# Kernel tuning notes

Measured on AMD Instinct MI355X. Metric: run time of the kernel, lower is better.

Reference implementation:

```python
import jax, jax.numpy as jnp
import numpy as np

EPS = 1e-5


def _rmsnorm(x, eps=EPS):
    return x * jax.lax.rsqrt(jnp.mean(x * x, axis=-1, keepdims=True) + eps)


def _bitlinear(x, w):
    # fla-style BitLinear: RMSNorm (no affine) -> 8-bit activation quant (STE)
    # -> ternary weight quant (STE) -> linear. w is [out, in].
    xn = _rmsnorm(x)
    s = 127.0 / jnp.clip(jnp.max(jnp.abs(xn), axis=-1, keepdims=True), 1e-5, None)
    xq = jnp.clip(jnp.round(xn * s), -128.0, 127.0) / s
    xq = xn + jax.lax.stop_gradient(xq - xn)
    ws = 1.0 / jnp.clip(jnp.mean(jnp.abs(w)), 1e-5, None)
    wq = jnp.clip(jnp.round(w * ws), -1.0, 1.0) / ws
    wq = w + jax.lax.stop_gradient(wq - w)
    return jnp.einsum('bld,od->blo', xq, wq)


def _hgrn_scan(i, f):
    # h_t = f_t * h_{t-1} + i_t along axis=2 (seq), h_0 = 0.
    def combine(a, b):
        fa, ia = a
        fb, ib = b
        return fa * fb, ia * fb + ib
    _, h = jax.lax.associative_scan(combine, (f, i), axis=2)
    return h


def _forward(hidden_states, Wi, Wf, Wg, Wo, g_norm_weight, num_heads=1):
    b, l, d = hidden_states.shape
    i = _bitlinear(hidden_states, Wi)
    f = jax.nn.sigmoid(_bitlinear(hidden_states, Wf))
    i = jax.nn.silu(i) * (1.0 - f)  # swiglu(i, 1-f)
    # [b, l, (h d)] -> [b, h, l, d_head]
    i = i.reshape(b, l, num_heads, -1).transpose(0, 2, 1, 3)
    f = f.reshape(b, l, num_heads, -1).transpose(0, 2, 1, 3)
    h = _hgrn_scan(i, f)
    h = h.transpose(0, 2, 1, 3).reshape(b, l, d)
    # FusedRMSNormSwishGate: rmsnorm(g)*weight * h*sigmoid(h)
    g = _bitlinear(hidden_states, Wg)
    o = _rmsnorm(g) * g_norm_weight * (h * jax.nn.sigmoid(h))
    return _bitlinear(o, Wo)


def setup_inputs() -> dict:
    key = jax.random.key(0)
    ks = jax.random.split(key, 5)
    B, L, D = 4, 2048, 2048
    gain = 2 ** (-2.5) * (6.0 / (2 * D)) ** 0.5  # xavier_uniform with gain 2^-2.5
    def w(k):
        return jax.random.uniform(k, (D, D), jnp.float32, -gain, gain)
    return {
        'hidden_states': jax.random.normal(ks[0], (B, L, D), jnp.float32),
        'Wi': w(ks[1]),
        'Wf': w(ks[2]),
        'Wg': w(ks[3]),
        'Wo': w(ks[4]),
        'g_norm_weight': jnp.ones((D,), jnp.float32),
    }


def reference(hidden_states, Wi, Wf, Wg, Wo, g_norm_weight):
    return _forward(hidden_states, Wi, Wf, Wg, Wo, g_norm_weight)
```

## Files before the change

### kernel.cpp

```cpp
#include <hip/hip_runtime.h>
#include <stdint.h>

#define B_DIM 4
#define L_DIM 2048
#define D_DIM 2048
#define M_DIM 8192
#define K_DIM 2048
#define N_DIM 2048
#define WELEM (D_DIM * D_DIM)
#define CHUNK 32
#define NCH (L_DIM / CHUNK)

typedef int v4i __attribute__((ext_vector_type(4)));
typedef unsigned short bfraw;

#define AS1 __attribute__((address_space(1)))
#define AS3 __attribute__((address_space(3)))

__device__ __forceinline__ void gl_lds16(const void* g, void* l) {
    __builtin_amdgcn_global_load_lds((AS1 void*)g, (AS3 void*)l, 16, 0, 0);
}

__device__ __forceinline__ float sigmoidf_(float x) { return 1.0f / (1.0f + expf(-x)); }

__device__ __forceinline__ float bf2f(bfraw u) {
    union { unsigned int i; float f; } c; c.i = ((unsigned int)u) << 16; return c.f;
}
__device__ __forceinline__ bfraw f2bf(float f) {
    union { float f; unsigned int i; } c; c.f = f;
    unsigned int lsb = (c.i >> 16) & 1;
    c.i += 0x7fffu + lsb;
    return (bfraw)(c.i >> 16);
}

__device__ __forceinline__ void store_out(float* p, float v) { *p = v; }
__device__ __forceinline__ void store_out(bfraw* p, float v) { *p = f2bf(v); }

__device__ __forceinline__ float block_sum256(float v) {
#pragma unroll
    for (int off = 32; off > 0; off >>= 1) v += __shfl_down(v, off);
    __shared__ float sb[4];
    int lane = threadIdx.x & 63, wv = threadIdx.x >> 6;
    __syncthreads();
    if (lane == 0) sb[wv] = v;
    __syncthreads();
    return sb[0] + sb[1] + sb[2] + sb[3];
}

__device__ __forceinline__ void block_sum_max256(float& s, float& m) {
#pragma unroll
    for (int off = 32; off > 0; off >>= 1) {
        s += __shfl_down(s, off);
        m = fmaxf(m, __shfl_down(m, off));
    }
    __shared__ float sb2[8];
    int lane = threadIdx.x & 63, wv = threadIdx.x >> 6;
    __syncthreads();
    if (lane == 0) { sb2[wv] = s; sb2[4 + wv] = m; }
    __syncthreads();
    s = sb2[0] + sb2[1] + sb2[2] + sb2[3];
    m = fmaxf(fmaxf(sb2[4], sb2[5]), fmaxf(sb2[6], sb2[7]));
}

__global__ void wstats1(const float* __restrict__ w0, const float* __restrict__ w1,
                        const float* __restrict__ w2, const float* __restrict__ w3,
                        float* __restrict__ wpart) {
    int w = blockIdx.x >> 7;
    int slice = blockIdx.x & 127;
    const float* W = (w == 0) ? w0 : ((w == 1) ? w1 : ((w == 2) ? w2 : w3));
    const float4* p = (const float4*)(W + (size_t)slice * (WELEM / 128));
    float s = 0.f;
    for (int i = threadIdx.x; i < (WELEM / 128 / 4); i += 256) {
        float4 v = p[i];
        s += fabsf(v.x) + fabsf(v.y) + fabsf(v.z) + fabsf(v.w);
    }
    s = block_sum256(s);
    if (threadIdx.x == 0) wpart[blockIdx.x] = s;
}

__global__ void wstats2(const float* __restrict__ wpart, float* __restrict__ wdeq) {
    int w = threadIdx.x >> 6;
    int lane = threadIdx.x & 63;
    float s = wpart[w * 128 + lane] + wpart[w * 128 + 64 + lane];
#pragma unroll
    for (int off = 32; off > 0; off >>= 1) s += __shfl_down(s, off);
    if (lane == 0) wdeq[w] = fmaxf(s * (1.0f / (float)WELEM), 1e-5f);
}

__global__ void quant_all(const float* __restrict__ w0, const float* __restrict__ w1,
                          const float* __restrict__ w2, const float* __restrict__ w3,
                          const float* __restrict__ wdeq, int8_t* __restrict__ wq,
                          const float* __restrict__ x, int8_t* __restrict__ xq,
                          float* __restrict__ adeq) {
    if (blockIdx.x < 16384) {
        size_t idx = (size_t)blockIdx.x * 256 + threadIdx.x;
        int w = (int)(idx >> 20);
        size_t g = idx & ((1u << 20) - 1);
        const float* W = (w == 0) ? w0 : ((w == 1) ? w1 : ((w == 2) ? w2 : w3));
        float inv = 1.0f / wdeq[w];
        float4 v = ((const float4*)W)[g];
        int q0 = (int)rintf(v.x * inv); q0 = q0 < -1 ? -1 : (q0 > 1 ? 1 : q0);
        int q1 = (int)rintf(v.y * inv); q1 = q1 < -1 ? -1 : (q1 > 1 ? 1 : q1);
        int q2 = (int)rintf(v.z * inv); q2 = q2 < -1 ? -1 : (q2 > 1 ? 1 : q2);
        int q3 = (int)rintf(v.w * inv); q3 = q3 < -1 ? -1 : (q3 > 1 ? 1 : q3);
        uint32_t p = (uint32_t)(q0 & 0xff) | ((uint32_t)(q1 & 0xff) << 8) |
                     ((uint32_t)(q2 & 0xff) << 16) | ((uint32_t)(q3 & 0xff) << 24);
        ((uint32_t*)(wq + (size_t)w * WELEM))[g] = p;
        return;
    }
    int row = blockIdx.x - 16384, tid = threadIdx.x;
    const float4* xr = (const float4*)(x + (size_t)row * D_DIM);
    float4 a = xr[2 * tid], b = xr[2 * tid + 1];
    float v[8] = {a.x, a.y, a.z, a.w, b.x, b.y, b.z, b.w};
    float ss = 0.f, mx = 0.f;
#pragma unroll
    for (int j = 0; j < 8; j++) { ss += v[j] * v[j]; mx = fmaxf(mx, fabsf(v[j])); }
    block_sum_max256(ss, mx);
    float inv = rsqrtf(ss * (1.0f / (float)D_DIM) + 1e-5f);
    float anc = fmaxf(mx * inv, 1e-5f);
    float s = 127.0f / anc;
    if (tid == 0) adeq[row] = anc * (1.0f / 127.0f);
    float sc = inv * s;
    int q[8];
#pragma unroll
    for (int j = 0; j < 8; j++) {
        int t = (int)rintf(v[j] * sc);
        q[j] = t < -128 ? -128 : (t > 127 ? 127 : t);
    }
    uint32_t lo = (uint32_t)(q[0] & 0xff) | ((uint32_t)(q[1] & 0xff) << 8) |
                  ((uint32_t)(q[2] & 0xff) << 16) | ((uint32_t)(q[3] & 0xff) << 24);
    uint32_t hi = (uint32_t)(q[4] & 0xff) | ((uint32_t)(q[5] & 0xff) << 8) |
                  ((uint32_t)(q[6] & 0xff) << 16) | ((uint32_t)(q[7] & 0xff) << 24);
    ((uint2*)(xq + (size_t)row * D_DIM))[tid] = make_uint2(lo, hi);
}

#define BM 128
#define BN 256
#define BKB 64

template <typename OutT>
__device__ __forceinline__ void gemm_core(
    const int8_t* __restrict__ A, const int8_t* __restrict__ Bw,
    const float* __restrict__ adeq, float wsc,
    int m0, int n0, OutT* __restrict__ Cout) {
    __shared__ int8_t sA[BM * BKB];
    __shared__ int8_t sB[BN * BKB];
    int lane = threadIdx.x & 63;
    int wv = threadIdx.x >> 6;
    int wm = (wv & 1) * 64;
    int wn = (wv >> 1) * 128;

    const v4i vzero = {0, 0, 0, 0};
    v4i acc[4][8];
#pragma unroll
    for (int i = 0; i < 4; i++)
#pragma unroll
        for (int j = 0; j < 8; j++) acc[i][j] = vzero;

    int rS = lane >> 2;
    int cS = (lane & 3) * 16;
    const int8_t* Ablk = A + (size_t)m0 * K_DIM;
    const int8_t* Bblk = Bw + (size_t)n0 * K_DIM;
    int qq = lane >> 4;
    int mr = lane & 15;

    for (int kt = 0; kt < K_DIM; kt += BKB) {
        gl_lds16(Ablk + (size_t)(wv * 16 + rS) * K_DIM + kt + cS, sA + (wv * 16) * BKB);
        gl_lds16(Ablk + (size_t)(64 + wv * 16 + rS) * K_DIM + kt + cS, sA + (64 + wv * 16) * BKB);
#pragma unroll
        for (int g = 0; g < 4; g++) {
            int rb = g * 64 + wv * 16;
            gl_lds16(Bblk + (size_t)(rb + rS) * K_DIM + kt + cS, sB + rb * BKB);
        }
        __syncthreads();

        v4i afrag[4], bfrag[8];
#pragma unroll
        for (int i = 0; i < 4; i++)
            afrag[i] = *(const v4i*)(sA + (size_t)(wm + i * 16 + mr) * BKB + qq * 16);
#pragma unroll
        for (int j = 0; j < 8; j++)
            bfrag[j] = *(const v4i*)(sB + (size_t)(wn + j * 16 + mr) * BKB + qq * 16);
#pragma unroll
        for (int i = 0; i < 4; i++)
#pragma unroll
            for (int j = 0; j < 8; j++)
                acc[i][j] = __builtin_amdgcn_mfma_i32_16x16x64_i8(afrag[i], bfrag[j], acc[i][j], 0, 0, 0);
        __syncthreads();
    }

    int cc = lane & 15;
#pragma unroll
    for (int i = 0; i < 4; i++) {
#pragma unroll
        for (int r = 0; r < 4; r++) {
            int row = m0 + wm + i * 16 + qq * 4 + r;
            float rs = adeq[row] * wsc;
            OutT* crow = Cout + (size_t)row * N_DIM + n0 + wn + cc;
#pragma unroll
            for (int j = 0; j < 8; j++) store_out(crow + j * 16, (float)acc[i][j][r] * rs);
        }
    }
}

__global__ __launch_bounds__(256, 2) void gemm_ifg(
    const int8_t* __restrict__ xq, const int8_t* __restrict__ wq,
    const float* __restrict__ adeq, const float* __restrict__ wdeq,
    bfraw* __restrict__ bufI, bfraw* __restrict__ bufF, bfraw* __restrict__ bufG) {
    int widx = blockIdx.x >> 3;
    int n0 = (blockIdx.x & 7) * BN;
    int m0 = blockIdx.y * BM;
    bfraw* outp = (widx == 0) ? bufI : ((widx == 1) ? bufF : bufG);
    gemm_core<bfraw>(xq, wq + (size_t)widx * WELEM, adeq, wdeq[widx], m0, n0, outp);
}

__global__ __launch_bounds__(256, 2) void gemm_o(
    const int8_t* __restrict__ oq, const int8_t* __restrict__ wq,
    const float* __restrict__ odeq, const float* __restrict__ wdeq,
    float* __restrict__ out) {
    gemm_core<float>(oq, wq + 3 * (size_t)WELEM, odeq, wdeq[3], blockIdx.y * BM,
                     blockIdx.x * BN, out);
}

__global__ void scan1(const bfraw* __restrict__ iL, const bfraw* __restrict__ fL,
                      float* __restrict__ Fc, float* __restrict__ Ic) {
    int idx = blockIdx.x * 256 + threadIdx.x;
    int d = idx & (D_DIM - 1);
    int c = (idx >> 11) & (NCH - 1);
    int b = idx >> 17;
    size_t base = ((size_t)(b * L_DIM + c * CHUNK)) * D_DIM + d;
    float F = 1.f, h = 0.f;
#pragma unroll 4
    for (int t = 0; t < CHUNK; t++) {
        float fr = bf2f(fL[base + (size_t)t * D_DIM]);
        float ir = bf2f(iL[base + (size_t)t * D_DIM]);
        float fv = sigmoidf_(fr);
        float iv = ir * sigmoidf_(ir) * (1.0f - fv);
        h = fv * h + iv;
        F *= fv;
    }
    size_t ci = ((size_t)b * NCH + c) * D_DIM + d;
    Fc[ci] = F;
    Ic[ci] = h;
}

__global__ void scan2(const float* __restrict__ Fc, const float* __restrict__ Ic,
                      float* __restrict__ Hc) {
    int idx = blockIdx.x * 256 + threadIdx.x;
    int d = idx & (D_DIM - 1);
    int b = idx >> 11;
    float h = 0.f;
    for (int c0 = 0; c0 < NCH; c0 += 8) {
        float F[8], I[8];
#pragma unroll
        for (int j = 0; j < 8; j++) {
            size_t ci = ((size_t)b * NCH + c0 + j) * D_DIM + d;
            F[j] = Fc[ci];
            I[j] = Ic[ci];
        }
#pragma unroll
        for (int j = 0; j < 8; j++) {
            size_t ci = ((size_t)b * NCH + c0 + j) * D_DIM + d;
            Hc[ci] = h;
            h = F[j] * h + I[j];
        }
    }
}

__global__ void scan3(const bfraw* __restrict__ iL, const bfraw* __restrict__ fL,
                      const float* __restrict__ Hc, bfraw* __restrict__ hout) {
    int idx = blockIdx.x * 256 + threadIdx.x;
    int d = idx & (D_DIM - 1);
    int c = (idx >> 11) & (NCH - 1);
    int b = idx >> 17;
    size_t base = ((size_t)(b * L_DIM + c * CHUNK)) * D_DIM + d;
    float h = Hc[((size_t)b * NCH + c) * D_DIM + d];
#pragma unroll 4
    for (int t = 0; t < CHUNK; t++) {
        size_t a = base + (size_t)t * D_DIM;
        float fr = bf2f(fL[a]);
        float ir = bf2f(iL[a]);
        float fv = sigmoidf_(fr);
        float iv = ir * sigmoidf_(ir) * (1.0f - fv);
        h = fv * h + iv;
        hout[a] = f2bf(h);
    }
}

union BF8 { uint4 u; bfraw s[8]; };

__global__ void gout_quant(const bfraw* __restrict__ gL, const bfraw* __restrict__ h,
                           const float* __restrict__ gw, int8_t* __restrict__ oq,
                           float* __restrict__ odeq) {
    int row = blockIdx.x, tid = threadIdx.x;
    BF8 g8, h8;
    g8.u = ((const uint4*)(gL + (size_t)row * D_DIM))[tid];
    float gv[8];
    float ss = 0.f;
#pragma unroll
    for (int j = 0; j < 8; j++) { gv[j] = bf2f(g8.s[j]); ss += gv[j] * gv[j]; }
    float ssg = block_sum256(ss);
    float invg = rsqrtf(ssg * (1.0f / (float)D_DIM) + 1e-5f);

    h8.u = ((const uint4*)(h + (size_t)row * D_DIM))[tid];
    const float4* wr = (const float4*)gw;
    float4 w0 = wr[2 * tid], w1 = wr[2 * tid + 1];
    float wv[8] = {w0.x, w0.y, w0.z, w0.w, w1.x, w1.y, w1.z, w1.w};
    float o[8];
    float sso = 0.f, amax = 0.f;
#pragma unroll
    for (int j = 0; j < 8; j++) {
        float hv = bf2f(h8.s[j]);
        o[j] = gv[j] * invg * wv[j] * hv * sigmoidf_(hv);
        sso += o[j] * o[j];
        amax = fmaxf(amax, fabsf(o[j]));
    }
    block_sum_max256(sso, amax);
    float invo = rsqrtf(sso * (1.0f / (float)D_DIM) + 1e-5f);
    float anc = fmaxf(amax * invo, 1e-5f);
    float s = 127.0f / anc;
    if (tid == 0) odeq[row] = anc * (1.0f / 127.0f);
    float sc = invo * s;
    int q[8];
#pragma unroll
    for (int j = 0; j < 8; j++) {
        int t = (int)rintf(o[j] * sc);
        q[j] = t < -128 ? -128 : (t > 127 ? 127 : t);
    }
    uint32_t lo = (uint32_t)(q[0] & 0xff) | ((uint32_t)(q[1] & 0xff) << 8) |
                  ((uint32_t)(q[2] & 0xff) << 16) | ((uint32_t)(q[3] & 0xff) << 24);
    uint32_t hi = (uint32_t)(q[4] & 0xff) | ((uint32_t)(q[5] & 0xff) << 8) |
                  ((uint32_t)(q[6] & 0xff) << 16) | ((uint32_t)(q[7] & 0xff) << 24);
    ((uint2*)(oq + (size_t)row * D_DIM))[tid] = make_uint2(lo, hi);
}

extern "C" void kernel_launch(void* const* d_in, const int* in_sizes, int n_in,
                              void* d_out, int out_size, void* d_ws, size_t ws_size,
                              hipStream_t stream) {
    const float* x  = (const float*)d_in[0];
    const float* Wi = (const float*)d_in[1];
    const float* Wf = (const float*)d_in[2];
    const float* Wg = (const float*)d_in[3];
    const float* Wo = (const float*)d_in[4];
    const float* gw = (const float*)d_in[5];
    float* out = (float*)d_out;

    char* ws = (char*)d_ws;
    float*  wdeq  = (float*)(ws + 0);
    float*  wpart = (float*)(ws + 256);
    float*  adeq  = (float*)(ws + 0x10000);
    float*  odeq  = (float*)(ws + 0x20000);
    int8_t* xq    = (int8_t*)(ws + 0x100000);
    int8_t* wq    = (int8_t*)(ws + 0x1100000);
    float*  Fc    = (float*)(ws + 0x2100000);
    float*  Ic    = (float*)(ws + 0x2300000);
    float*  Hc    = (float*)(ws + 0x2500000);
    bfraw*  bufI  = (bfraw*)(ws + 0x4000000);
    bfraw*  bufF  = (bfraw*)(ws + 0x6000000);
    bfraw*  bufG  = (bfraw*)(ws + 0x8000000);
    bfraw*  hbuf  = (bfraw*)(ws + 0xA000000);

    wstats1<<<512, 256, 0, stream>>>(Wi, Wf, Wg, Wo, wpart);
    wstats2<<<1, 256, 0, stream>>>(wpart, wdeq);
    quant_all<<<16384 + 8192, 256, 0, stream>>>(Wi, Wf, Wg, Wo, wdeq, wq, x, xq, adeq);

    gemm_ifg<<<dim3(24, M_DIM / BM), 256, 0, stream>>>(xq, wq, adeq, wdeq, bufI, bufF, bufG);

    scan1<<<2048, 256, 0, stream>>>(bufI, bufF, Fc, Ic);
    scan2<<<32, 256, 0, stream>>>(Fc, Ic, Hc);
    scan3<<<2048, 256, 0, stream>>>(bufI, bufF, Hc, hbuf);

    gout_quant<<<M_DIM, 256, 0, stream>>>(bufG, hbuf, gw, xq , odeq);
    gemm_o<<<dim3(N_DIM / BN, M_DIM / BM), 256, 0, stream>>>(xq , wq, odeq, wdeq, out);

    (void)in_sizes; (void)n_in; (void)out_size; (void)ws_size;
}
```

Measured before the change: 430.9 us.

## Fuse pipeline into one cooperative persistent kernel with grid syncs and swizzled LDS

All stages (weight stats, quantization, the three input GEMMs, the chunked scan, the gated norm plus quant, and the output GEMM) move into one cooperative persistent kernel with 512 or 256 blocks, separated by grid.sync. The separate kernels are kept as a fallback if the cooperative launch fails. The GEMM LDS layout also gets an XOR swizzle on 16-byte columns to reduce bank conflicts. This removes launch gaps between nine kernels, but the persistent grid caps GEMM parallelism at the resident block count, ties every stage to the GEMM's register and LDS footprint, and adds grid-sync cost.

```diff
diff --git a/kernel.cpp b/kernel.cpp
--- a/kernel.cpp
+++ b/kernel.cpp
@@ -1,5 +1,8 @@
 #include <hip/hip_runtime.h>
+#include <hip/hip_cooperative_groups.h>
 #include <stdint.h>
+
+namespace cg = cooperative_groups;
 
 #define B_DIM 4
 #define L_DIM 2048
@@ -11,6 +14,10 @@
 #define CHUNK 32
 #define NCH (L_DIM / CHUNK)
 
+#define BM 128
+#define BN 256
+#define BKB 64
+
 typedef int v4i __attribute__((ext_vector_type(4)));
 typedef unsigned short bfraw;
 
@@ -36,10 +43,9 @@
 __device__ __forceinline__ void store_out(float* p, float v) { *p = v; }
 __device__ __forceinline__ void store_out(bfraw* p, float v) { *p = f2bf(v); }
 
-__device__ __forceinline__ float block_sum256(float v) {
+__device__ __forceinline__ float block_sum256(float v, float* sb) {
 #pragma unroll
     for (int off = 32; off > 0; off >>= 1) v += __shfl_down(v, off);
-    __shared__ float sb[4];
     int lane = threadIdx.x & 63, wv = threadIdx.x >> 6;
     __syncthreads();
     if (lane == 0) sb[wv] = v;
@@ -47,57 +53,47 @@
     return sb[0] + sb[1] + sb[2] + sb[3];
 }
 
-__device__ __forceinline__ void block_sum_max256(float& s, float& m) {
+__device__ __forceinline__ void block_sum_max256(float& s, float& m, float* sb) {
 #pragma unroll
     for (int off = 32; off > 0; off >>= 1) {
         s += __shfl_down(s, off);
         m = fmaxf(m, __shfl_down(m, off));
     }
-    __shared__ float sb2[8];
     int lane = threadIdx.x & 63, wv = threadIdx.x >> 6;
     __syncthreads();
-    if (lane == 0) { sb2[wv] = s; sb2[4 + wv] = m; }
+    if (lane == 0) { sb[wv] = s; sb[4 + wv] = m; }
     __syncthreads();
-    s = sb2[0] + sb2[1] + sb2[2] + sb2[3];
-    m = fmaxf(fmaxf(sb2[4], sb2[5]), fmaxf(sb2[6], sb2[7]));
-}
-
-__global__ void wstats1(const float* __restrict__ w0, const float* __restrict__ w1,
-                        const float* __restrict__ w2, const float* __restrict__ w3,
-                        float* __restrict__ wpart) {
-    int w = blockIdx.x >> 7;
-    int slice = blockIdx.x & 127;
-    const float* W = (w == 0) ? w0 : ((w == 1) ? w1 : ((w == 2) ? w2 : w3));
+    s = sb[0] + sb[1] + sb[2] + sb[3];
+    m = fmaxf(fmaxf(sb[4], sb[5]), fmaxf(sb[6], sb[7]));
+}
+
+
+__device__ __forceinline__ void wstats1_body(int u, const float* Wi, const float* Wf,
+                                             const float* Wg, const float* Wo,
+                                             float* wpart, float* red) {
+    int w = u >> 7, slice = u & 127;
+    const float* W = (w == 0) ? Wi : ((w == 1) ? Wf : ((w == 2) ? Wg : Wo));
     const float4* p = (const float4*)(W + (size_t)slice * (WELEM / 128));
     float s = 0.f;
     for (int i = threadIdx.x; i < (WELEM / 128 / 4); i += 256) {
         float4 v = p[i];
         s += fabsf(v.x) + fabsf(v.y) + fabsf(v.z) + fabsf(v.w);
     }
-    s = block_sum256(s);
-    if (threadIdx.x == 0) wpart[blockIdx.x] = s;
-}
-
-__global__ void wstats2(const float* __restrict__ wpart, float* __restrict__ wdeq) {
-    int w = threadIdx.x >> 6;
-    int lane = threadIdx.x & 63;
-    float s = wpart[w * 128 + lane] + wpart[w * 128 + 64 + lane];
-#pragma unroll
-    for (int off = 32; off > 0; off >>= 1) s += __shfl_down(s, off);
-    if (lane == 0) wdeq[w] = fmaxf(s * (1.0f / (float)WELEM), 1e-5f);
-}
-
-__global__ void quant_all(const float* __restrict__ w0, const float* __restrict__ w1,
-                          const float* __restrict__ w2, const float* __restrict__ w3,
-                          const float* __restrict__ wdeq, int8_t* __restrict__ wq,
-                          const float* __restrict__ x, int8_t* __restrict__ xq,
-                          float* __restrict__ adeq) {
-    if (blockIdx.x < 16384) {
-        size_t idx = (size_t)blockIdx.x * 256 + threadIdx.x;
-        int w = (int)(idx >> 20);
-        size_t g = idx & ((1u << 20) - 1);
-        const float* W = (w == 0) ? w0 : ((w == 1) ? w1 : ((w == 2) ? w2 : w3));
-        float inv = 1.0f / wdeq[w];
+    s = block_sum256(s, red);
+    if (threadIdx.x == 0) wpart[u] = s;
+}
+
+__device__ __forceinline__ void quant_body(int unit, const float* Wi, const float* Wf,
+                                           const float* Wg, const float* Wo,
+                                           const float* wdq, int8_t* wq,
+                                           const float* x, int8_t* xq, float* adeq,
+                                           float* red) {
+    int tid = threadIdx.x;
+    if (unit < 16384) {
+        int w = unit >> 12;
+        size_t g = ((size_t)(unit & 4095)) * 256 + tid;
+        const float* W = (w == 0) ? Wi : ((w == 1) ? Wf : ((w == 2) ? Wg : Wo));
+        float inv = 1.0f / wdq[w];
         float4 v = ((const float4*)W)[g];
         int q0 = (int)rintf(v.x * inv); q0 = q0 < -1 ? -1 : (q0 > 1 ? 1 : q0);
         int q1 = (int)rintf(v.y * inv); q1 = q1 < -1 ? -1 : (q1 > 1 ? 1 : q1);
@@ -108,14 +104,14 @@
         ((uint32_t*)(wq + (size_t)w * WELEM))[g] = p;
         return;
     }
-    int row = blockIdx.x - 16384, tid = threadIdx.x;
+    int row = unit - 16384;
     const float4* xr = (const float4*)(x + (size_t)row * D_DIM);
     float4 a = xr[2 * tid], b = xr[2 * tid + 1];
     float v[8] = {a.x, a.y, a.z, a.w, b.x, b.y, b.z, b.w};
     float ss = 0.f, mx = 0.f;
 #pragma unroll
     for (int j = 0; j < 8; j++) { ss += v[j] * v[j]; mx = fmaxf(mx, fabsf(v[j])); }
-    block_sum_max256(ss, mx);
+    block_sum_max256(ss, mx, red);
     float inv = rsqrtf(ss * (1.0f / (float)D_DIM) + 1e-5f);
     float anc = fmaxf(mx * inv, 1e-5f);
     float s = 127.0f / anc;
@@ -134,19 +130,14 @@
     ((uint2*)(xq + (size_t)row * D_DIM))[tid] = make_uint2(lo, hi);
 }
 
-#define BM 128
-#define BN 256
-#define BKB 64
-
 template <typename OutT>
-__device__ __forceinline__ void gemm_core(
-    const int8_t* __restrict__ A, const int8_t* __restrict__ Bw,
-    const float* __restrict__ adeq, float wsc,
-    int m0, int n0, OutT* __restrict__ Cout) {
-    __shared__ int8_t sA[BM * BKB];
-    __shared__ int8_t sB[BN * BKB];
-    int lane = threadIdx.x & 63;
-    int wv = threadIdx.x >> 6;
+__device__ void gemm_core(const int8_t* A, const int8_t* Bw,
+                          const float* adeq, float wsc,
+                          int m0, int n0, OutT* Cout,
+                          int8_t* sA, int8_t* sB) {
+    int tid = threadIdx.x;
+    int lane = tid & 63;
+    int wv = tid >> 6;
     int wm = (wv & 1) * 64;
     int wn = (wv >> 1) * 128;
 
@@ -158,29 +149,30 @@
         for (int j = 0; j < 8; j++) acc[i][j] = vzero;
 
     int rS = lane >> 2;
-    int cS = (lane & 3) * 16;
+    int swz = (((lane & 3) ^ (rS & 3)) << 4);
     const int8_t* Ablk = A + (size_t)m0 * K_DIM;
     const int8_t* Bblk = Bw + (size_t)n0 * K_DIM;
     int qq = lane >> 4;
     int mr = lane & 15;
+    int roff = ((qq ^ (mr & 3)) << 4);
 
     for (int kt = 0; kt < K_DIM; kt += BKB) {
-        gl_lds16(Ablk + (size_t)(wv * 16 + rS) * K_DIM + kt + cS, sA + (wv * 16) * BKB);
-        gl_lds16(Ablk + (size_t)(64 + wv * 16 + rS) * K_DIM + kt + cS, sA + (64 + wv * 16) * BKB);
+        gl_lds16(Ablk + (size_t)(wv * 16 + rS) * K_DIM + kt + swz, sA + (wv * 16) * BKB);
+        gl_lds16(Ablk + (size_t)(64 + wv * 16 + rS) * K_DIM + kt + swz, sA + (64 + wv * 16) * BKB);
 #pragma unroll
         for (int g = 0; g < 4; g++) {
             int rb = g * 64 + wv * 16;
-            gl_lds16(Bblk + (size_t)(rb + rS) * K_DIM + kt + cS, sB + rb * BKB);
+            gl_lds16(Bblk + (size_t)(rb + rS) * K_DIM + kt + swz, sB + rb * BKB);
         }
         __syncthreads();
 
         v4i afrag[4], bfrag[8];
 #pragma unroll
         for (int i = 0; i < 4; i++)
-            afrag[i] = *(const v4i*)(sA + (size_t)(wm + i * 16 + mr) * BKB + qq * 16);
+            afrag[i] = *(const v4i*)(sA + (size_t)(wm + i * 16 + mr) * BKB + roff);
 #pragma unroll
         for (int j = 0; j < 8; j++)
-            bfrag[j] = *(const v4i*)(sB + (size_t)(wn + j * 16 + mr) * BKB + qq * 16);
+            bfrag[j] = *(const v4i*)(sB + (size_t)(wn + j * 16 + mr) * BKB + roff);
 #pragma unroll
         for (int i = 0; i < 4; i++)
 #pragma unroll
@@ -203,28 +195,8 @@
     }
 }
 
-__global__ __launch_bounds__(256, 2) void gemm_ifg(
-    const int8_t* __restrict__ xq, const int8_t* __restrict__ wq,
-    const float* __restrict__ adeq, const float* __restrict__ wdeq,
-    bfraw* __restrict__ bufI, bfraw* __restrict__ bufF, bfraw* __restrict__ bufG) {
-    int widx = blockIdx.x >> 3;
-    int n0 = (blockIdx.x & 7) * BN;
-    int m0 = blockIdx.y * BM;
-    bfraw* outp = (widx == 0) ? bufI : ((widx == 1) ? bufF : bufG);
-    gemm_core<bfraw>(xq, wq + (size_t)widx * WELEM, adeq, wdeq[widx], m0, n0, outp);
-}
-
-__global__ __launch_bounds__(256, 2) void gemm_o(
-    const int8_t* __restrict__ oq, const int8_t* __restrict__ wq,
-    const float* __restrict__ odeq, const float* __restrict__ wdeq,
-    float* __restrict__ out) {
-    gemm_core<float>(oq, wq + 3 * (size_t)WELEM, odeq, wdeq[3], blockIdx.y * BM,
-                     blockIdx.x * BN, out);
-}
-
-__global__ void scan1(const bfraw* __restrict__ iL, const bfraw* __restrict__ fL,
-                      float* __restrict__ Fc, float* __restrict__ Ic) {
-    int idx = blockIdx.x * 256 + threadIdx.x;
+__device__ __forceinline__ void scan1_body(int idx, const bfraw* bufI, const bfraw* bufF,
+                                           float* Fc, float* Ic) {
     int d = idx & (D_DIM - 1);
     int c = (idx >> 11) & (NCH - 1);
     int b = idx >> 17;
@@ -232,8 +204,8 @@
     float F = 1.f, h = 0.f;
 #pragma unroll 4
     for (int t = 0; t < CHUNK; t++) {
-        float fr = bf2f(fL[base + (size_t)t * D_DIM]);
-        float ir = bf2f(iL[base + (size_t)t * D_DIM]);
+        float fr = bf2f(bufF[base + (size_t)t * D_DIM]);
+        float ir = bf2f(bufI[base + (size_t)t * D_DIM]);
         float fv = sigmoidf_(fr);
         float iv = ir * sigmoidf_(ir) * (1.0f - fv);
         h = fv * h + iv;
@@ -244,11 +216,10 @@
     Ic[ci] = h;
 }
 
-__global__ void scan2(const float* __restrict__ Fc, const float* __restrict__ Ic,
-                      float* __restrict__ Hc) {
-    int idx = blockIdx.x * 256 + threadIdx.x;
-    int d = idx & (D_DIM - 1);
-    int b = idx >> 11;
+__device__ __forceinline__ void scan2_body(int gt, const float* Fc, const float* Ic,
+                                           float* Hc) {
+    int d = gt & (D_DIM - 1);
+    int b = gt >> 11;
     float h = 0.f;
     for (int c0 = 0; c0 < NCH; c0 += 8) {
         float F[8], I[8];
@@ -267,9 +238,8 @@
     }
 }
 
-__global__ void scan3(const bfraw* __restrict__ iL, const bfraw* __restrict__ fL,
-                      const float* __restrict__ Hc, bfraw* __restrict__ hout) {
-    int idx = blockIdx.x * 256 + threadIdx.x;
+__device__ __forceinline__ void scan3_body(int idx, const bfraw* bufI, const bfraw* bufF,
+                                           const float* Hc, bfraw* hbuf) {
     int d = idx & (D_DIM - 1);
     int c = (idx >> 11) & (NCH - 1);
     int b = idx >> 17;
@@ -278,44 +248,42 @@
 #pragma unroll 4
     for (int t = 0; t < CHUNK; t++) {
         size_t a = base + (size_t)t * D_DIM;
-        float fr = bf2f(fL[a]);
-        float ir = bf2f(iL[a]);
+        float fr = bf2f(bufF[a]);
+        float ir = bf2f(bufI[a]);
         float fv = sigmoidf_(fr);
         float iv = ir * sigmoidf_(ir) * (1.0f - fv);
         h = fv * h + iv;
-        hout[a] = f2bf(h);
-    }
-}
-
-union BF8 { uint4 u; bfraw s[8]; };
-
-__global__ void gout_quant(const bfraw* __restrict__ gL, const bfraw* __restrict__ h,
-                           const float* __restrict__ gw, int8_t* __restrict__ oq,
-                           float* __restrict__ odeq) {
-    int row = blockIdx.x, tid = threadIdx.x;
-    BF8 g8, h8;
-    g8.u = ((const uint4*)(gL + (size_t)row * D_DIM))[tid];
+        hbuf[a] = f2bf(h);
+    }
+}
+
+__device__ __forceinline__ void gout_body(int row, const bfraw* bufG, const bfraw* hbuf,
+                                          const float* gw, int8_t* oq, float* odeq,
+                                          float* red) {
+    int tid = threadIdx.x;
+    union { uint4 u; bfraw s[8]; } g8, h8;
+    g8.u = ((const uint4*)(bufG + (size_t)row * D_DIM))[tid];
     float gv[8];
     float ss = 0.f;
 #pragma unroll
     for (int j = 0; j < 8; j++) { gv[j] = bf2f(g8.s[j]); ss += gv[j] * gv[j]; }
-    float ssg = block_sum256(ss);
+    float ssg = block_sum256(ss, red);
     float invg = rsqrtf(ssg * (1.0f / (float)D_DIM) + 1e-5f);
 
-    h8.u = ((const uint4*)(h + (size_t)row * D_DIM))[tid];
+    h8.u = ((const uint4*)(hbuf + (size_t)row * D_DIM))[tid];
     const float4* wr = (const float4*)gw;
     float4 w0 = wr[2 * tid], w1 = wr[2 * tid + 1];
-    float wv[8] = {w0.x, w0.y, w0.z, w0.w, w1.x, w1.y, w1.z, w1.w};
+    float wv8[8] = {w0.x, w0.y, w0.z, w0.w, w1.x, w1.y, w1.z, w1.w};
     float o[8];
     float sso = 0.f, amax = 0.f;
 #pragma unroll
     for (int j = 0; j < 8; j++) {
         float hv = bf2f(h8.s[j]);
-        o[j] = gv[j] * invg * wv[j] * hv * sigmoidf_(hv);
+        o[j] = gv[j] * invg * wv8[j] * hv * sigmoidf_(hv);
         sso += o[j] * o[j];
         amax = fmaxf(amax, fabsf(o[j]));
     }
-    block_sum_max256(sso, amax);
+    block_sum_max256(sso, amax, red);
     float invo = rsqrtf(sso * (1.0f / (float)D_DIM) + 1e-5f);
     float anc = fmaxf(amax * invo, 1e-5f);
     float s = 127.0f / anc;
@@ -332,6 +300,141 @@
     uint32_t hi = (uint32_t)(q[4] & 0xff) | ((uint32_t)(q[5] & 0xff) << 8) |
                   ((uint32_t)(q[6] & 0xff) << 16) | ((uint32_t)(q[7] & 0xff) << 24);
     ((uint2*)(oq + (size_t)row * D_DIM))[tid] = make_uint2(lo, hi);
+}
+
+template <int NB>
+__global__ __launch_bounds__(256, 2) void hgrn_fused(
+    const float* x, const float* Wi, const float* Wf, const float* Wg, const float* Wo,
+    const float* gw, float* wpart, float* adeq, float* odeq,
+    int8_t* xq, int8_t* wq, float* Fc, float* Ic, float* Hc,
+    bfraw* bufI, bfraw* bufF, bfraw* bufG, bfraw* hbuf, float* out) {
+    cg::grid_group grid = cg::this_grid();
+    __shared__ union {
+        struct { int8_t A[BM * BKB]; int8_t B[BN * BKB]; } g;
+        float red[16];
+    } sm;
+
+    const int bid = blockIdx.x;
+    const int tid = threadIdx.x;
+    const int lane = tid & 63, wvi = tid >> 6;
+
+    for (int u = bid; u < 512; u += NB)
+        wstats1_body(u, Wi, Wf, Wg, Wo, wpart, sm.red);
+    grid.sync();
+
+    float wdq[4];
+    {
+        float s = wpart[wvi * 128 + lane] + wpart[wvi * 128 + 64 + lane];
+#pragma unroll
+        for (int off = 32; off > 0; off >>= 1) s += __shfl_down(s, off);
+        __syncthreads();
+        if (lane == 0) sm.red[wvi] = fmaxf(s * (1.0f / (float)WELEM), 1e-5f);
+        __syncthreads();
+        wdq[0] = sm.red[0]; wdq[1] = sm.red[1]; wdq[2] = sm.red[2]; wdq[3] = sm.red[3];
+        __syncthreads();
+    }
+
+    for (int unit = bid; unit < 24576; unit += NB)
+        quant_body(unit, Wi, Wf, Wg, Wo, wdq, wq, x, xq, adeq, sm.red);
+    grid.sync();
+
+    for (int t = bid; t < 1536; t += NB) {
+        int r = t >> 9;
+        int tt = t & 511;
+        int m0 = (tt & 63) * BM;
+        int n0 = (tt >> 6) * BN;
+        bfraw* outp = (r == 0) ? bufI : ((r == 1) ? bufF : bufG);
+        gemm_core<bfraw>(xq, wq + (size_t)r * WELEM, adeq, wdq[r], m0, n0, outp,
+                         sm.g.A, sm.g.B);
+    }
+    grid.sync();
+
+    for (int u = bid * 256 + tid; u < 524288; u += NB * 256)
+        scan1_body(u, bufI, bufF, Fc, Ic);
+    grid.sync();
+
+    {
+        int gt = bid * 256 + tid;
+        if (gt < 8192) scan2_body(gt, Fc, Ic, Hc);
+    }
+    grid.sync();
+
+    for (int u = bid * 256 + tid; u < 524288; u += NB * 256)
+        scan3_body(u, bufI, bufF, Hc, hbuf);
+    grid.sync();
+
+    for (int row = bid; row < 8192; row += NB)
+        gout_body(row, bufG, hbuf, gw, xq, odeq, sm.red);
+    grid.sync();
+
+    for (int t = bid; t < 512; t += NB) {
+        int m0 = (t & 63) * BM;
+        int n0 = (t >> 6) * BN;
+        gemm_core<float>(xq, wq + 3 * (size_t)WELEM, odeq, wdq[3], m0, n0, out,
+                         sm.g.A, sm.g.B);
+    }
+}
+
+__global__ void k_wstats1(const float* Wi, const float* Wf, const float* Wg,
+                          const float* Wo, float* wpart) {
+    __shared__ float red[16];
+    wstats1_body(blockIdx.x, Wi, Wf, Wg, Wo, wpart, red);
+}
+
+__global__ void k_wstats2(const float* __restrict__ wpart, float* __restrict__ wdeq) {
+    int w = threadIdx.x >> 6;
+    int lane = threadIdx.x & 63;
+    float s = wpart[w * 128 + lane] + wpart[w * 128 + 64 + lane];
+#pragma unroll
+    for (int off = 32; off > 0; off >>= 1) s += __shfl_down(s, off);
+    if (lane == 0) wdeq[w] = fmaxf(s * (1.0f / (float)WELEM), 1e-5f);
+}
+
+__global__ void k_quant(const float* Wi, const float* Wf, const float* Wg,
+                        const float* Wo, const float* wdeq, int8_t* wq,
+                        const float* x, int8_t* xq, float* adeq) {
+    __shared__ float red[16];
+    quant_body(blockIdx.x, Wi, Wf, Wg, Wo, wdeq, wq, x, xq, adeq, red);
+}
+
+__global__ __launch_bounds__(256, 2) void k_gemm_ifg(
+    const int8_t* xq, const int8_t* wq, const float* adeq, const float* wdeq,
+    bfraw* bufI, bfraw* bufF, bfraw* bufG) {
+    __shared__ int8_t sA[BM * BKB];
+    __shared__ int8_t sB[BN * BKB];
+    int widx = blockIdx.x >> 3;
+    int n0 = (blockIdx.x & 7) * BN;
+    int m0 = blockIdx.y * BM;
+    bfraw* outp = (widx == 0) ? bufI : ((widx == 1) ? bufF : bufG);
+    gemm_core<bfraw>(xq, wq + (size_t)widx * WELEM, adeq, wdeq[widx], m0, n0, outp, sA, sB);
+}
+
+__global__ __launch_bounds__(256, 2) void k_gemm_o(
+    const int8_t* oq, const int8_t* wq, const float* odeq, const float* wdeq,
+    float* out) {
+    __shared__ int8_t sA[BM * BKB];
+    __shared__ int8_t sB[BN * BKB];
+    gemm_core<float>(oq, wq + 3 * (size_t)WELEM, odeq, wdeq[3], blockIdx.y * BM,
+                     blockIdx.x * BN, out, sA, sB);
+}
+
+__global__ void k_scan1(const bfraw* bufI, const bfraw* bufF, float* Fc, float* Ic) {
+    scan1_body(blockIdx.x * 256 + threadIdx.x, bufI, bufF, Fc, Ic);
+}
+
+__global__ void k_scan2(const float* Fc, const float* Ic, float* Hc) {
+    scan2_body(blockIdx.x * 256 + threadIdx.x, Fc, Ic, Hc);
+}
+
+__global__ void k_scan3(const bfraw* bufI, const bfraw* bufF, const float* Hc,
+                        bfraw* hbuf) {
+    scan3_body(blockIdx.x * 256 + threadIdx.x, bufI, bufF, Hc, hbuf);
+}
+
+__global__ void k_gout(const bfraw* bufG, const bfraw* hbuf, const float* gw,
+                       int8_t* oq, float* odeq) {
+    __shared__ float red[16];
+    gout_body(blockIdx.x, bufG, hbuf, gw, oq, odeq, red);
 }
 
 extern "C" void kernel_launch(void* const* d_in, const int* in_sizes, int n_in,
@@ -346,8 +449,8 @@
     float* out = (float*)d_out;
 
     char* ws = (char*)d_ws;
-    float*  wdeq  = (float*)(ws + 0);
-    float*  wpart = (float*)(ws + 256);
+    float*  wpart = (float*)(ws + 0);
+    float*  wdeq  = (float*)(ws + 0x8000);
     float*  adeq  = (float*)(ws + 0x10000);
     float*  odeq  = (float*)(ws + 0x20000);
     int8_t* xq    = (int8_t*)(ws + 0x100000);
@@ -360,18 +463,38 @@
     bfraw*  bufG  = (bfraw*)(ws + 0x8000000);
     bfraw*  hbuf  = (bfraw*)(ws + 0xA000000);
 
-    wstats1<<<512, 256, 0, stream>>>(Wi, Wf, Wg, Wo, wpart);
-    wstats2<<<1, 256, 0, stream>>>(wpart, wdeq);
-    quant_all<<<16384 + 8192, 256, 0, stream>>>(Wi, Wf, Wg, Wo, wdeq, wq, x, xq, adeq);
-
-    gemm_ifg<<<dim3(24, M_DIM / BM), 256, 0, stream>>>(xq, wq, adeq, wdeq, bufI, bufF, bufG);
-
-    scan1<<<2048, 256, 0, stream>>>(bufI, bufF, Fc, Ic);
-    scan2<<<32, 256, 0, stream>>>(Fc, Ic, Hc);
-    scan3<<<2048, 256, 0, stream>>>(bufI, bufF, Hc, hbuf);
-
-    gout_quant<<<M_DIM, 256, 0, stream>>>(bufG, hbuf, gw, xq , odeq);
-    gemm_o<<<dim3(N_DIM / BN, M_DIM / BM), 256, 0, stream>>>(xq , wq, odeq, wdeq, out);
+    void* args[] = {
+        (void*)&x, (void*)&Wi, (void*)&Wf, (void*)&Wg, (void*)&Wo, (void*)&gw,
+        (void*)&wpart, (void*)&adeq, (void*)&odeq,
+        (void*)&xq, (void*)&wq, (void*)&Fc, (void*)&Ic, (void*)&Hc,
+        (void*)&bufI, (void*)&bufF, (void*)&bufG, (void*)&hbuf, (void*)&out
+    };
+
+    hipError_t rc = hipErrorUnknown;
+    int mab512 = 0, mab256 = 0;
+    (void)hipOccupancyMaxActiveBlocksPerMultiprocessor(&mab512, hgrn_fused<512>, 256, 0);
+    (void)hipOccupancyMaxActiveBlocksPerMultiprocessor(&mab256, hgrn_fused<256>, 256, 0);
+    if (mab512 >= 2) {
+        rc = hipLaunchCooperativeKernel((const void*)hgrn_fused<512>, dim3(512),
+                                        dim3(256), args, 0, stream);
+    } else if (mab256 >= 1) {
+        rc = hipLaunchCooperativeKernel((const void*)hgrn_fused<256>, dim3(256),
+                                        dim3(256), args, 0, stream);
+    }
+
+    if (rc != hipSuccess) {
+        k_wstats1<<<512, 256, 0, stream>>>(Wi, Wf, Wg, Wo, wpart);
+        k_wstats2<<<1, 256, 0, stream>>>(wpart, wdeq);
+        k_quant<<<24576, 256, 0, stream>>>(Wi, Wf, Wg, Wo, wdeq, wq, x, xq, adeq);
+        k_gemm_ifg<<<dim3(24, M_DIM / BM), 256, 0, stream>>>(xq, wq, adeq, wdeq,
+                                                             bufI, bufF, bufG);
+        k_scan1<<<2048, 256, 0, stream>>>(bufI, bufF, Fc, Ic);
+        k_scan2<<<32, 256, 0, stream>>>(Fc, Ic, Hc);
+        k_scan3<<<2048, 256, 0, stream>>>(bufI, bufF, Hc, hbuf);
+        k_gout<<<M_DIM, 256, 0, stream>>>(bufG, hbuf, gw, xq , odeq);
+        k_gemm_o<<<dim3(N_DIM / BN, M_DIM / BM), 256, 0, stream>>>(xq , wq,
+                                                                   odeq, wdeq, out);
+    }
 
     (void)in_sizes; (void)n_in; (void)out_size; (void)ws_size;
 }
```

Result: slower. 961.4 us (+123.1%).
